# Optimization experiments

Measured on AMD Instinct MI355X. Metric: run time of the kernel, lower is better.

Reference implementation:

```python
import jax, jax.numpy as jnp
import numpy as np

EPS = 1e-8
TAU = 0.2
IOU_THR = 0.5
NEG = -1e9
N, C, H, D_FG, D_CLS = 8192, 1024, 256, 64, 128


def setup_inputs() -> dict:
    key = jax.random.key(0)
    ks = jax.random.split(key, 11)
    def lin(k, fan_in, fan_out):
        return jax.random.normal(k, (fan_in, fan_out), jnp.float32) / np.sqrt(fan_in)
    return {
        "roi_feats": jax.random.normal(ks[0], (N, C), jnp.float32),
        "labels": jax.random.randint(ks[1], (N,), 0, 21, jnp.int32).astype(jnp.int64),
        "ious": jax.random.uniform(ks[2], (N,), jnp.float32),
        "fg_w1": lin(ks[3], C, H), "fg_b1": jnp.zeros((H,), jnp.float32),
        "fg_w2": lin(ks[4], H, D_FG), "fg_b2": jnp.zeros((D_FG,), jnp.float32),
        "cls_w1": lin(ks[5], C, H), "cls_b1": jnp.zeros((H,), jnp.float32),
        "cls_w2": lin(ks[6], H, D_CLS), "cls_b2": jnp.zeros((D_CLS,), jnp.float32),
    }


def _project_normalize(x, w1, b1, w2, b2):
    h = jax.nn.relu(x @ w1 + b1)
    z = h @ w2 + b2
    norm = jnp.maximum(jnp.linalg.norm(z, axis=1, keepdims=True), EPS)
    return z / norm


def _forward(roi_feats, labels, ious, fg_w1, fg_b1, fg_w2, fg_b2, cls_w1, cls_b1, cls_w2, cls_b2):
    n = roi_feats.shape[0]
    z_fg = _project_normalize(roi_feats, fg_w1, fg_b1, fg_w2, fg_b2)
    z_cls = _project_normalize(roi_feats, cls_w1, cls_b1, cls_w2, cls_b2)

    ignore = labels == -1
    fg = (labels > 0) & ~ignore
    iou_weight = jnp.where(ious > IOU_THR, ious, 0.0)
    eye = jnp.eye(n, dtype=bool)

    # ---- fg/bg contrastive (bg_as_negatives_only=True) ----
    sim_fg = (z_fg @ z_fg.T) / TAU                       # [N,N]
    exp_sim = jnp.exp(sim_fg)
    denom = jnp.sum(exp_sim * (~eye).astype(jnp.float32), axis=1)
    pos = (fg & ~ignore)[None, :] & ~eye                 # positives: fg columns, no self
    n_pos = jnp.sum(pos, axis=1)
    numer = jnp.sum(exp_sim * pos.astype(jnp.float32), axis=1)
    # original computes den = denom + EPS then -log((numer+EPS)/(den+EPS))
    loss_i = -jnp.log((numer + EPS) / (denom + 2.0 * EPS))
    valid = (fg & ~ignore) & (n_pos > 0)
    w = iou_weight * valid.astype(jnp.float32)
    loss_fg_bg = jnp.sum(w * loss_i) / (jnp.sum(w) + EPS)

    # ---- class supervised contrastive ----
    sim_cls = (z_cls @ z_cls.T) / TAU
    sim_masked = jnp.where(eye, NEG, sim_cls)
    log_denom = jax.nn.logsumexp(sim_masked, axis=1)     # [N]
    log_p = jnp.where(eye, NEG, sim_cls - log_denom[:, None])
    # pos_mask keeps diagonal (as in original): same label, col not ignore, col label != 0
    posc = (labels[None, :] == labels[:, None]) & (~ignore)[None, :] & (labels[None, :] != 0)
    n_posc = jnp.sum(posc, axis=1).astype(jnp.float32)
    sum_log_p = jnp.sum(log_p * posc.astype(jnp.float32), axis=1)
    valid_c = (fg & ~ignore) & (n_posc > 0) & jnp.isfinite(log_denom)
    Lzi = jnp.where(valid_c, -sum_log_p / (n_posc + EPS), 0.0)
    wc = iou_weight * valid_c.astype(jnp.float32)
    loss_supcon = jnp.sum(wc * Lzi) / (jnp.sum(wc) + EPS)

    return jnp.stack([loss_fg_bg, loss_supcon])


def reference(roi_feats, labels, ious, fg_w1, fg_b1, fg_w2, fg_b2, cls_w1, cls_b1, cls_w2, cls_b2):
    return _forward(roi_feats, labels, ious, fg_w1, fg_b1, fg_w2, fg_b2, cls_w1, cls_b1, cls_w2, cls_b2)
```

## Files before the change

kernel.cpp:

```cpp
#include <hip/hip_runtime.h>


typedef __attribute__((ext_vector_type(8))) short bs8;
typedef __attribute__((ext_vector_type(4))) float f4;

#define MFMA_BF16(a, b, c) __builtin_amdgcn_mfma_f32_16x16x32_bf16((a), (b), (c), 0, 0, 0)

#if defined(__has_builtin)
#if __has_builtin(__builtin_amdgcn_exp2f)
#define EXP2F(x) __builtin_amdgcn_exp2f(x)
#endif
#endif
#ifndef EXP2F
#define EXP2F(x) exp2f(x)
#endif

#define K_LOG2E 7.2134752044448170f

__device__ __forceinline__ unsigned short f2bf(float f) {
  unsigned int u = __float_as_uint(f);
  u = (u + 0x7fffu + ((u >> 16) & 1u)) >> 16;
  return (unsigned short)u;
}
__device__ __forceinline__ float bf2f(unsigned short s) {
  return __uint_as_float(((unsigned int)s) << 16);
}

constexpr size_t O_W1T  = 0;
constexpr size_t O_W2TF = 1048576;
constexpr size_t O_W2TC = 1081344;
constexpr size_t O_H    = 1146880;
constexpr size_t O_ZF   = 9535488;
constexpr size_t O_ZC   = 10584064;
constexpr size_t O_SCLS = 12681216;
constexpr size_t O_ROWD = 12697600;
constexpr size_t O_ROWN = 12730368;
constexpr size_t O_ROWS = 12763136;
constexpr size_t O_SCAL = 12795904;
constexpr size_t O_HIST = 12795920;
constexpr size_t O_NFG  = 12796048;
constexpr int ZERO_WORDS = (int)((O_SCAL + 16 - O_SCLS) / 4);

__global__ void __launch_bounds__(256) prep_kernel(
    const float* __restrict__ fgw1, const float* __restrict__ clsw1,
    const float* __restrict__ fgw2, const float* __restrict__ clsw2,
    const int* __restrict__ labels,
    unsigned short* __restrict__ W1T, unsigned short* __restrict__ W2Tf,
    unsigned short* __restrict__ W2Tc,
    int* __restrict__ hist, int* __restrict__ nfg, float* __restrict__ zp) {
  const int b = blockIdx.x;
  const int t = threadIdx.x;

  if (b >= 141) {
    const int i = (b - 141) * 256 + t;
    if (i < ZERO_WORDS) zp[i] = 0.f;
    return;
  }
  if (b == 140) {
    __shared__ int sh[33];
    if (t < 33) sh[t] = 0;
    __syncthreads();
    for (int it = 0; it < 32; it++) {
      const int lab = labels[it * 256 + t];
      if (lab >= 0 && lab < 32) atomicAdd(&sh[lab], 1);
      if (lab > 0) atomicAdd(&sh[32], 1);
    }
    __syncthreads();
    if (t < 32) hist[t] = sh[t];
    if (t == 32) *nfg = sh[32];
    return;
  }
  int m, tb;
  if (b < 64)       { m = 0; tb = b; }
  else if (b < 128) { m = 1; tb = b - 64; }
  else if (b < 132) { m = 2; tb = b - 128; }
  else              { m = 3; tb = b - 132; }
  __shared__ float tile[64][65];
  const float* src;
  unsigned short* dst;
  int R, C;
  if (m == 0)      { src = fgw1;  dst = W1T;              R = 1024; C = 256; }
  else if (m == 1) { src = clsw1; dst = W1T + 256 * 1024; R = 1024; C = 256; }
  else if (m == 2) { src = fgw2;  dst = W2Tf;             R = 256;  C = 64;  }
  else             { src = clsw2; dst = W2Tc;             R = 256;  C = 128; }
  const int cT = C >> 6;
  const int r0 = (tb / cT) << 6, c0 = (tb % cT) << 6;
  {
    const int rr = t >> 4, cc = (t & 15) << 2;
#pragma unroll
    for (int i = 0; i < 4; i++) {
      float4 v = *(const float4*)(src + (size_t)(r0 + rr + i * 16) * C + c0 + cc);
      tile[rr + i * 16][cc] = v.x; tile[rr + i * 16][cc + 1] = v.y;
      tile[rr + i * 16][cc + 2] = v.z; tile[rr + i * 16][cc + 3] = v.w;
    }
  }
  __syncthreads();
  {
    const int dr = t >> 2, dc = (t & 3) << 4;
    bs8 o0, o1;
#pragma unroll
    for (int j = 0; j < 8; j++) o0[j] = (short)f2bf(tile[dc + j][dr]);
#pragma unroll
    for (int j = 0; j < 8; j++) o1[j] = (short)f2bf(tile[dc + 8 + j][dr]);
    unsigned short* dp = dst + (size_t)(c0 + dr) * R + r0 + dc;
    *(bs8*)dp = o0;
    *(bs8*)(dp + 8) = o1;
  }
}

__global__ void __launch_bounds__(512) gemm1_kernel(
    const float* __restrict__ X, const unsigned short* __restrict__ W1T,
    const float* __restrict__ b1f, const float* __restrict__ b1c,
    unsigned short* __restrict__ H) {
  __shared__ __align__(16) unsigned short lA[64 * 72];
  __shared__ __align__(16) unsigned short lB[128 * 72];
  const int t = threadIdx.x;
  const int w = t >> 6, lane = t & 63, ln = lane & 15, quad = lane >> 4;
  const int wr = (w & 3) * 16, wc = (w >> 2) * 64;
  const int m0 = blockIdx.x * 64, n0 = blockIdx.y * 128;

  const int ar = t >> 3, ac = (t & 7) * 8;
  const int br = t >> 2, bc = (t & 3) * 16;
  const float* xbase = X + (size_t)(m0 + ar) * 1024 + ac;
  const unsigned short* bbase = W1T + (size_t)(n0 + br) * 1024 + bc;

  float4 xa[2];
  bs8 xb[2];
#pragma unroll
  for (int i = 0; i < 2; i++) xa[i] = *(const float4*)(xbase + i * 4);
#pragma unroll
  for (int i = 0; i < 2; i++) xb[i] = *(const bs8*)(bbase + i * 8);

  f4 acc[4];
#pragma unroll
  for (int s = 0; s < 4; s++) acc[s] = (f4){0.f, 0.f, 0.f, 0.f};

  for (int ks = 0; ks < 16; ks++) {
    {
      bs8 av;
      av[0] = (short)f2bf(xa[0].x); av[1] = (short)f2bf(xa[0].y);
      av[2] = (short)f2bf(xa[0].z); av[3] = (short)f2bf(xa[0].w);
      av[4] = (short)f2bf(xa[1].x); av[5] = (short)f2bf(xa[1].y);
      av[6] = (short)f2bf(xa[1].z); av[7] = (short)f2bf(xa[1].w);
      *(bs8*)&lA[ar * 72 + ac] = av;
      unsigned short* bp = &lB[br * 72 + bc];
      *(bs8*)(bp) = xb[0];
      *(bs8*)(bp + 8) = xb[1];
    }
    __syncthreads();
    if (ks < 15) {
      const int k1 = (ks + 1) * 64;
#pragma unroll
      for (int i = 0; i < 2; i++) xa[i] = *(const float4*)(xbase + k1 + i * 4);
#pragma unroll
      for (int i = 0; i < 2; i++) xb[i] = *(const bs8*)(bbase + k1 + i * 8);
    }
#pragma unroll
    for (int kk = 0; kk < 2; kk++) {
      bs8 af = *(const bs8*)&lA[(wr + ln) * 72 + kk * 32 + quad * 8];
#pragma unroll
      for (int s = 0; s < 4; s++) {
        bs8 bf = *(const bs8*)&lB[(wc + s * 16 + ln) * 72 + kk * 32 + quad * 8];
        acc[s] = MFMA_BF16(af, bf, acc[s]);
      }
    }
    __syncthreads();
  }
#pragma unroll
  for (int s = 0; s < 4; s++) {
    const int n = n0 + wc + s * 16 + ln;
    const float b = (n < 256) ? b1f[n] : b1c[n - 256];
#pragma unroll
    for (int r = 0; r < 4; r++) {
      float v = fmaxf(acc[s][r] + b, 0.f);
      H[(size_t)(m0 + wr + quad * 4 + r) * 512 + n] = f2bf(v);
    }
  }
}

__global__ void __launch_bounds__(256) gemm2_kernel(
    const unsigned short* __restrict__ H,
    const unsigned short* __restrict__ W2Tf, const unsigned short* __restrict__ W2Tc,
    const float* __restrict__ b2f, const float* __restrict__ b2c,
    unsigned short* __restrict__ Zf, unsigned short* __restrict__ Zc) {
  const int t = threadIdx.x;
  const int w = t >> 6, lane = t & 63, ln = lane & 15, quad = lane >> 4;
  const int rw = blockIdx.x * 32 + (w & 1) * 16;

  if (w < 2) {
    const unsigned short* hrow = H + (size_t)(rw + ln) * 512;
    f4 acc[4];
#pragma unroll
    for (int s = 0; s < 4; s++) acc[s] = (f4){0.f, 0.f, 0.f, 0.f};
#pragma unroll
    for (int ks = 0; ks < 8; ks++) {
      bs8 af = *(const bs8*)(hrow + ks * 32 + quad * 8);
#pragma unroll
      for (int s = 0; s < 4; s++) {
        bs8 bf = *(const bs8*)(W2Tf + (size_t)(s * 16 + ln) * 256 + ks * 32 + quad * 8);
        acc[s] = MFMA_BF16(af, bf, acc[s]);
      }
    }
    float ss[4] = {0.f, 0.f, 0.f, 0.f};
#pragma unroll
    for (int s = 0; s < 4; s++) {
      float b = b2f[s * 16 + ln];
#pragma unroll
      for (int r = 0; r < 4; r++) {
        acc[s][r] += b;
        ss[r] = fmaf(acc[s][r], acc[s][r], ss[r]);
      }
    }
#pragma unroll
    for (int r = 0; r < 4; r++) {
#pragma unroll
      for (int off = 1; off < 16; off <<= 1) ss[r] += __shfl_xor(ss[r], off, 64);
      float sc = 1.f / fmaxf(sqrtf(ss[r]), 1e-8f);
#pragma unroll
      for (int s = 0; s < 4; s++)
        Zf[(size_t)(rw + quad * 4 + r) * 64 + s * 16 + ln] = f2bf(acc[s][r] * sc);
    }
  } else {
    const unsigned short* hrow = H + (size_t)(rw + ln) * 512 + 256;
    f4 acc[8];
#pragma unroll
    for (int s = 0; s < 8; s++) acc[s] = (f4){0.f, 0.f, 0.f, 0.f};
#pragma unroll
    for (int ks = 0; ks < 8; ks++) {
      bs8 af = *(const bs8*)(hrow + ks * 32 + quad * 8);
#pragma unroll
      for (int s = 0; s < 8; s++) {
        bs8 bf = *(const bs8*)(W2Tc + (size_t)(s * 16 + ln) * 256 + ks * 32 + quad * 8);
        acc[s] = MFMA_BF16(af, bf, acc[s]);
      }
    }
    float ss[4] = {0.f, 0.f, 0.f, 0.f};
#pragma unroll
    for (int s = 0; s < 8; s++) {
      float b = b2c[s * 16 + ln];
#pragma unroll
      for (int r = 0; r < 4; r++) {
        acc[s][r] += b;
        ss[r] = fmaf(acc[s][r], acc[s][r], ss[r]);
      }
    }
#pragma unroll
    for (int r = 0; r < 4; r++) {
#pragma unroll
      for (int off = 1; off < 16; off <<= 1) ss[r] += __shfl_xor(ss[r], off, 64);
      float sc = 1.f / fmaxf(sqrtf(ss[r]), 1e-8f);
#pragma unroll
      for (int s = 0; s < 8; s++)
        Zc[(size_t)(rw + quad * 4 + r) * 128 + s * 16 + ln] = f2bf(acc[s][r] * sc);
    }
  }
}

__global__ void __launch_bounds__(128) scls_kernel(const unsigned short* __restrict__ Zc,
                                                   const int* __restrict__ labels,
                                                   float* __restrict__ Scls) {
  const int c = blockIdx.x + 1;
  const int t = threadIdx.x;
  const int r0 = blockIdx.y * 256;
  float acc = 0.f;
#pragma unroll 4
  for (int r = r0; r < r0 + 256; r++) {
    if (labels[r] == c) acc += bf2f(Zc[(size_t)r * 128 + t]);
  }
  atomicAdd(&Scls[c * 128 + t], acc);
}

__global__ void __launch_bounds__(256) sim2_kernel(
    const unsigned short* __restrict__ Zf, const unsigned short* __restrict__ Zc,
    const int* __restrict__ labels,
    float* __restrict__ rowD, float* __restrict__ rowN, float* __restrict__ rowS) {
  const int bi = blockIdx.x, y = blockIdx.y;
  const bool isfg = (y < 9);
  const int y2 = isfg ? y : y - 9;
  int dlo, dhi;
  if (y2 == 0)      { dlo = 0;      dhi = 3;      }
  else if (y2 < 8)  { dlo = y2 * 4; dhi = y2 * 4 + 3; }
  else              { dlo = 32;     dhi = 32; if (bi >= 32) return; }

  __shared__ __align__(16) char arena[19456];
  const int t = threadIdx.x;
  const int w = t >> 6, lane = t & 63, ln = lane & 15, quad = lane >> 4;
  const int rbase = bi * 128 + w * 32;

  if (isfg) {
    unsigned short* sZf = (unsigned short*)arena;
    float* sFg = (float*)(arena + 9216);
    float* sCol = (float*)(arena + 9472);

    bs8 afg[2][2];
    float fgr[2][4];
#pragma unroll
    for (int rs = 0; rs < 2; rs++) {
      const unsigned short* zf = Zf + (size_t)(rbase + rs * 16 + ln) * 64;
#pragma unroll
      for (int s = 0; s < 2; s++) afg[rs][s] = *(const bs8*)(zf + s * 32 + quad * 8);
#pragma unroll
      for (int r = 0; r < 4; r++)
        fgr[rs][r] = (labels[rbase + rs * 16 + quad * 4 + r] > 0) ? 1.f : 0.f;
    }

    float dacc[2][4] = {}, nacc[2][4] = {};

    for (int d = dlo; d <= dhi; d++) {
      const int bj = (bi + d) & 63;
      float cd[2][4] = {}, cn[2][4] = {};

#pragma unroll
      for (int ct = 0; ct < 2; ct++) {
        const int c0 = bj * 128 + ct * 64;
        __syncthreads();
#pragma unroll
        for (int i = 0; i < 2; i++) {
          int ch = t + i * 256;
          int j = ch >> 3, c8 = (ch & 7) * 8;
          *(bs8*)&sZf[j * 72 + c8] = *(const bs8*)(Zf + (size_t)(c0 + j) * 64 + c8);
        }
        if (t < 64) sFg[t] = (labels[c0 + t] > 0) ? 1.f : 0.f;
        __syncthreads();

#pragma unroll
        for (int s = 0; s < 4; s++) {
          const int lcol = s * 16 + ln;
          const float fgc = sFg[lcol];
          bs8 b0 = *(const bs8*)&sZf[lcol * 72 + quad * 8];
          bs8 b1 = *(const bs8*)&sZf[lcol * 72 + 32 + quad * 8];
#pragma unroll
          for (int rs = 0; rs < 2; rs++) {
            f4 c = {0.f, 0.f, 0.f, 0.f};
            c = MFMA_BF16(afg[rs][0], b0, c);
            c = MFMA_BF16(afg[rs][1], b1, c);
#pragma unroll
            for (int r = 0; r < 4; r++) {
              float e = EXP2F(c[r] * K_LOG2E);
              dacc[rs][r] += e;
              nacc[rs][r] = fmaf(fgc, e, nacc[rs][r]);
              cd[ct][s] += e;
              cn[ct][s] = fmaf(fgr[rs][r], e, cn[ct][s]);
            }
          }
        }
      }

      if (d != 0) {
#pragma unroll
        for (int ct = 0; ct < 2; ct++)
#pragma unroll
          for (int s = 0; s < 4; s++) {
            float dv = cd[ct][s], nv = cn[ct][s];
#pragma unroll
            for (int off = 16; off < 64; off <<= 1) {
              dv += __shfl_xor(dv, off, 64);
              nv += __shfl_xor(nv, off, 64);
            }
            if (quad == 0) {
              const int idx = (((w * 2 + ct) * 4 + s) * 16 + ln) * 2;
              sCol[idx] = dv;
              sCol[idx + 1] = nv;
            }
          }
        __syncthreads();
        if (t < 128) {
          const int ct = t >> 6, s = (t >> 4) & 3, lm = t & 15;
          float dv = 0.f, nv = 0.f;
#pragma unroll
          for (int ww = 0; ww < 4; ww++) {
            const int idx = (((ww * 2 + ct) * 4 + s) * 16 + lm) * 2;
            dv += sCol[idx];
            nv += sCol[idx + 1];
          }
          const int col = bj * 128 + t;
          atomicAdd(&rowD[col], dv);
          atomicAdd(&rowN[col], nv);
        }
      }
    }

#pragma unroll
    for (int rs = 0; rs < 2; rs++)
#pragma unroll
      for (int r = 0; r < 4; r++) {
        float dv = dacc[rs][r], nv = nacc[rs][r];
#pragma unroll
        for (int off = 1; off < 16; off <<= 1) {
          dv += __shfl_xor(dv, off, 64);
          nv += __shfl_xor(nv, off, 64);
        }
        if (ln == 0) {
          int row = rbase + rs * 16 + quad * 4 + r;
          atomicAdd(&rowD[row], dv);
          atomicAdd(&rowN[row], nv);
        }
      }
  } else {
    unsigned short* sZc = (unsigned short*)arena;
    float* sCol = (float*)(arena + 17408);

    bs8 acl[2][4];
#pragma unroll
    for (int rs = 0; rs < 2; rs++) {
      const unsigned short* zc = Zc + (size_t)(rbase + rs * 16 + ln) * 128;
#pragma unroll
      for (int s = 0; s < 4; s++) acl[rs][s] = *(const bs8*)(zc + s * 32 + quad * 8);
    }

    float sacc[2][4] = {};

    for (int d = dlo; d <= dhi; d++) {
      const int bj = (bi + d) & 63;
      float cs[2][4] = {};

#pragma unroll
      for (int ct = 0; ct < 2; ct++) {
        const int c0 = bj * 128 + ct * 64;
        __syncthreads();
#pragma unroll
        for (int i = 0; i < 4; i++) {
          int ch = t + i * 256;
          int j = ch >> 4, c8 = (ch & 15) * 8;
          *(bs8*)&sZc[j * 136 + c8] = *(const bs8*)(Zc + (size_t)(c0 + j) * 128 + c8);
        }
        __syncthreads();

#pragma unroll
        for (int s = 0; s < 4; s++) {
          const int lcol = s * 16 + ln;
          bs8 bc0 = *(const bs8*)&sZc[lcol * 136 + quad * 8];
          bs8 bc1 = *(const bs8*)&sZc[lcol * 136 + 32 + quad * 8];
          bs8 bc2 = *(const bs8*)&sZc[lcol * 136 + 64 + quad * 8];
          bs8 bc3 = *(const bs8*)&sZc[lcol * 136 + 96 + quad * 8];
#pragma unroll
          for (int rs = 0; rs < 2; rs++) {
            f4 c = {0.f, 0.f, 0.f, 0.f};
            c = MFMA_BF16(acl[rs][0], bc0, c);
            c = MFMA_BF16(acl[rs][1], bc1, c);
            c = MFMA_BF16(acl[rs][2], bc2, c);
            c = MFMA_BF16(acl[rs][3], bc3, c);
#pragma unroll
            for (int r = 0; r < 4; r++) {
              float e = EXP2F(c[r] * K_LOG2E);
              sacc[rs][r] += e;
              cs[ct][s] += e;
            }
          }
        }
      }

      if (d != 0) {
#pragma unroll
        for (int ct = 0; ct < 2; ct++)
#pragma unroll
          for (int s = 0; s < 4; s++) {
            float sv = cs[ct][s];
#pragma unroll
            for (int off = 16; off < 64; off <<= 1) sv += __shfl_xor(sv, off, 64);
            if (quad == 0) sCol[((w * 2 + ct) * 4 + s) * 16 + ln] = sv;
          }
        __syncthreads();
        if (t < 128) {
          const int ct = t >> 6, s = (t >> 4) & 3, lm = t & 15;
          float sv = 0.f;
#pragma unroll
          for (int ww = 0; ww < 4; ww++) sv += sCol[((ww * 2 + ct) * 4 + s) * 16 + lm];
          atomicAdd(&rowS[bj * 128 + t], sv);
        }
      }
    }

#pragma unroll
    for (int rs = 0; rs < 2; rs++)
#pragma unroll
      for (int r = 0; r < 4; r++) {
        float sv = sacc[rs][r];
#pragma unroll
        for (int off = 1; off < 16; off <<= 1) sv += __shfl_xor(sv, off, 64);
        if (ln == 0)
          atomicAdd(&rowS[rbase + rs * 16 + quad * 4 + r], sv);
      }
  }
}

__global__ void __launch_bounds__(256) finalize_kernel(
    const unsigned short* __restrict__ Zf, const unsigned short* __restrict__ Zc,
    const int* __restrict__ labels, const float* __restrict__ ious,
    const float* __restrict__ rowD, const float* __restrict__ rowN,
    const float* __restrict__ rowS, const float* __restrict__ Scls,
    const int* __restrict__ hist, const int* __restrict__ nfg,
    float* __restrict__ scal) {
  __shared__ float red[4][4];
  const int t = threadIdx.x, w = t >> 6, lane = t & 63;
  float aw0 = 0.f, al0 = 0.f, aw1 = 0.f, al1 = 0.f;
  const int NFG = *nfg;
  for (int it = 0; it < 16; it++) {
    const int i = it * 512 + blockIdx.x * 4 + w;
    const int lab = labels[i];
    if (lab > 0 && lab < 32) {
      const float iou = ious[i];
      const float iw = (iou > 0.5f) ? iou : 0.f;
      float dot = 0.f, ssq = 0.f;
#pragma unroll
      for (int p = 0; p < 2; p++) {
        const int k = lane + p * 64;
        const float z = bf2f(Zc[(size_t)i * 128 + k]);
        dot = fmaf(z, Scls[lab * 128 + k], dot);
        ssq = fmaf(z, z, ssq);
      }
      float zf = bf2f(Zf[(size_t)i * 64 + lane]);
      float ssqf = zf * zf;
#pragma unroll
      for (int off = 1; off < 64; off <<= 1) {
        dot += __shfl_xor(dot, off, 64);
        ssq += __shfl_xor(ssq, off, 64);
        ssqf += __shfl_xor(ssqf, off, 64);
      }
      if (lane == 0) {
        const float ef = EXP2F(K_LOG2E * ssqf);
        if (NFG - 1 > 0) {
          const float D = rowD[i] - ef;
          const float Nn = rowN[i] - ef;
          const float loss = logf(D + 2e-8f) - logf(Nn + 1e-8f);
          aw0 += iw;
          al0 += iw * loss;
        }
        const int npc = hist[lab];
        if (npc > 0) {
          const float S = rowS[i] - EXP2F(K_LOG2E * ssq);
          const float logden = logf(S);
          const float slp = (dot - ssq) * 5.0f - (float)(npc - 1) * logden - 1e9f;
          aw1 += iw;
          al1 += iw * (-slp / ((float)npc + 1e-8f));
        }
      }
    }
  }
  if (lane == 0) { red[w][0] = aw0; red[w][1] = al0; red[w][2] = aw1; red[w][3] = al1; }
  __syncthreads();
  if (t < 4) atomicAdd(&scal[t], red[0][t] + red[1][t] + red[2][t] + red[3][t]);
}

__global__ void writeout_kernel(const float* __restrict__ scal, float* __restrict__ out) {
  if (threadIdx.x == 0) {
    out[0] = scal[1] / (scal[0] + 1e-8f);
    out[1] = scal[3] / (scal[2] + 1e-8f);
  }
}

extern "C" void kernel_launch(void* const* d_in, const int* in_sizes, int n_in,
                              void* d_out, int out_size, void* d_ws, size_t ws_size,
                              hipStream_t stream) {
  (void)in_sizes; (void)n_in; (void)out_size; (void)ws_size;
  const float* roi    = (const float*)d_in[0];
  const int*   labels = (const int*)d_in[1];
  const float* ious   = (const float*)d_in[2];
  const float* fgw1   = (const float*)d_in[3];
  const float* fgb1   = (const float*)d_in[4];
  const float* fgw2   = (const float*)d_in[5];
  const float* fgb2   = (const float*)d_in[6];
  const float* clsw1  = (const float*)d_in[7];
  const float* clsb1  = (const float*)d_in[8];
  const float* clsw2  = (const float*)d_in[9];
  const float* clsb2  = (const float*)d_in[10];

  char* ws = (char*)d_ws;
  unsigned short* W1T  = (unsigned short*)(ws + O_W1T);
  unsigned short* W2Tf = (unsigned short*)(ws + O_W2TF);
  unsigned short* W2Tc = (unsigned short*)(ws + O_W2TC);
  unsigned short* Hb   = (unsigned short*)(ws + O_H);
  unsigned short* Zf   = (unsigned short*)(ws + O_ZF);
  unsigned short* Zc   = (unsigned short*)(ws + O_ZC);
  float* Scls = (float*)(ws + O_SCLS);
  float* rowD = (float*)(ws + O_ROWD);
  float* rowN = (float*)(ws + O_ROWN);
  float* rowS = (float*)(ws + O_ROWS);
  float* scal = (float*)(ws + O_SCAL);
  int* hist = (int*)(ws + O_HIST);
  int* nfg  = (int*)(ws + O_NFG);
  float* out = (float*)d_out;

  hipLaunchKernelGGL(prep_kernel, dim3(254), dim3(256), 0, stream,
                     fgw1, clsw1, fgw2, clsw2, labels, W1T, W2Tf, W2Tc,
                     hist, nfg, (float*)(ws + O_SCLS));
  hipLaunchKernelGGL(gemm1_kernel, dim3(128, 4), dim3(512), 0, stream,
                     roi, W1T, fgb1, clsb1, Hb);
  hipLaunchKernelGGL(gemm2_kernel, dim3(256), dim3(256), 0, stream,
                     Hb, W2Tf, W2Tc, fgb2, clsb2, Zf, Zc);
  hipLaunchKernelGGL(scls_kernel, dim3(20, 32), dim3(128), 0, stream, Zc, labels, Scls);
  hipLaunchKernelGGL(sim2_kernel, dim3(64, 18), dim3(256), 0, stream,
                     Zf, Zc, labels, rowD, rowN, rowS);
  hipLaunchKernelGGL(finalize_kernel, dim3(128), dim3(256), 0, stream,
                     Zf, Zc, labels, ious, rowD, rowN, rowS, Scls, hist, nfg, scal);
  hipLaunchKernelGGL(writeout_kernel, dim3(1), dim3(64), 0, stream, scal, out);
}
```

Baseline: 205.1 us.

## Fuse class-sum accumulation into gemm2 and final writeout into finalize

Drops the separate scls_kernel: gemm2 now accumulates per-class sums of the normalized Zc rows in shared memory with LDS atomics and flushes nonzero entries to global Scls. It also removes writeout_kernel, using a last-block ticket counter in finalize_kernel to compute the output ratios. This saves two kernel launches and a re-read of Zc, at the cost of LDS atomics inside gemm2 and a counter placed inside the zeroed Scls region (class 31 slot), which depends on prep zeroing it each call.

New measurement: 201.6 us, median of 3. No clear change (-1.7%).

```diff
diff --git a/kernel.cpp b/kernel.cpp
--- a/kernel.cpp
+++ b/kernel.cpp
@@ -39,6 +39,7 @@
 constexpr size_t O_SCAL = 12795904;
 constexpr size_t O_HIST = 12795920;
 constexpr size_t O_NFG  = 12796048;
+constexpr size_t O_CNT  = O_SCLS + 31 * 128 * 4;
 constexpr int ZERO_WORDS = (int)((O_SCAL + 16 - O_SCLS) / 4);
 
 __global__ void __launch_bounds__(256) prep_kernel(
@@ -182,8 +183,14 @@
     const unsigned short* __restrict__ H,
     const unsigned short* __restrict__ W2Tf, const unsigned short* __restrict__ W2Tc,
     const float* __restrict__ b2f, const float* __restrict__ b2c,
-    unsigned short* __restrict__ Zf, unsigned short* __restrict__ Zc) {
+    const int* __restrict__ labels,
+    unsigned short* __restrict__ Zf, unsigned short* __restrict__ Zc,
+    float* __restrict__ Scls) {
+  __shared__ float sS[21 * 128];
   const int t = threadIdx.x;
+  for (int i = t; i < 21 * 128; i += 256) sS[i] = 0.f;
+  __syncthreads();
+
   const int w = t >> 6, lane = t & 63, ln = lane & 15, quad = lane >> 4;
   const int rw = blockIdx.x * 32 + (w & 1) * 16;
 
@@ -249,25 +256,21 @@
 #pragma unroll
       for (int off = 1; off < 16; off <<= 1) ss[r] += __shfl_xor(ss[r], off, 64);
       float sc = 1.f / fmaxf(sqrtf(ss[r]), 1e-8f);
-#pragma unroll
-      for (int s = 0; s < 8; s++)
-        Zc[(size_t)(rw + quad * 4 + r) * 128 + s * 16 + ln] = f2bf(acc[s][r] * sc);
-    }
-  }
-}
-
-__global__ void __launch_bounds__(128) scls_kernel(const unsigned short* __restrict__ Zc,
-                                                   const int* __restrict__ labels,
-                                                   float* __restrict__ Scls) {
-  const int c = blockIdx.x + 1;
-  const int t = threadIdx.x;
-  const int r0 = blockIdx.y * 256;
-  float acc = 0.f;
-#pragma unroll 4
-  for (int r = r0; r < r0 + 256; r++) {
-    if (labels[r] == c) acc += bf2f(Zc[(size_t)r * 128 + t]);
-  }
-  atomicAdd(&Scls[c * 128 + t], acc);
+      const int lab = labels[rw + quad * 4 + r];
+#pragma unroll
+      for (int s = 0; s < 8; s++) {
+        const unsigned short us = f2bf(acc[s][r] * sc);
+        Zc[(size_t)(rw + quad * 4 + r) * 128 + s * 16 + ln] = us;
+        if (lab > 0 && lab < 21) atomicAdd(&sS[lab * 128 + s * 16 + ln], bf2f(us));
+      }
+    }
+  }
+
+  __syncthreads();
+  for (int i = t; i < 20 * 128; i += 256) {
+    const float v = sS[128 + i];
+    if (v != 0.f) atomicAdd(&Scls[128 + i], v);
+  }
 }
 
 __global__ void __launch_bounds__(256) sim2_kernel(
@@ -490,7 +493,8 @@
     const float* __restrict__ rowD, const float* __restrict__ rowN,
     const float* __restrict__ rowS, const float* __restrict__ Scls,
     const int* __restrict__ hist, const int* __restrict__ nfg,
-    float* __restrict__ scal) {
+    float* __restrict__ scal, unsigned int* __restrict__ cnt,
+    float* __restrict__ out) {
   __shared__ float red[4][4];
   const int t = threadIdx.x, w = t >> 6, lane = t & 63;
   float aw0 = 0.f, al0 = 0.f, aw1 = 0.f, al1 = 0.f;
@@ -540,12 +544,19 @@
   if (lane == 0) { red[w][0] = aw0; red[w][1] = al0; red[w][2] = aw1; red[w][3] = al1; }
   __syncthreads();
   if (t < 4) atomicAdd(&scal[t], red[0][t] + red[1][t] + red[2][t] + red[3][t]);
-}
-
-__global__ void writeout_kernel(const float* __restrict__ scal, float* __restrict__ out) {
-  if (threadIdx.x == 0) {
-    out[0] = scal[1] / (scal[0] + 1e-8f);
-    out[1] = scal[3] / (scal[2] + 1e-8f);
+  __syncthreads();
+  if (t == 0) {
+    __threadfence();
+    const unsigned int ticket = atomicAdd(cnt, 1u);
+    if (ticket == gridDim.x - 1) {
+      __threadfence();
+      const float s0 = atomicAdd(&scal[0], 0.f);
+      const float s1 = atomicAdd(&scal[1], 0.f);
+      const float s2 = atomicAdd(&scal[2], 0.f);
+      const float s3 = atomicAdd(&scal[3], 0.f);
+      out[0] = s1 / (s0 + 1e-8f);
+      out[1] = s3 / (s2 + 1e-8f);
+    }
   }
 }
 
@@ -577,6 +588,7 @@
   float* rowN = (float*)(ws + O_ROWN);
   float* rowS = (float*)(ws + O_ROWS);
   float* scal = (float*)(ws + O_SCAL);
+  unsigned int* cnt = (unsigned int*)(ws + O_CNT);
   int* hist = (int*)(ws + O_HIST);
   int* nfg  = (int*)(ws + O_NFG);
   float* out = (float*)d_out;
@@ -587,11 +599,10 @@
   hipLaunchKernelGGL(gemm1_kernel, dim3(128, 4), dim3(512), 0, stream,
                      roi, W1T, fgb1, clsb1, Hb);
   hipLaunchKernelGGL(gemm2_kernel, dim3(256), dim3(256), 0, stream,
-                     Hb, W2Tf, W2Tc, fgb2, clsb2, Zf, Zc);
-  hipLaunchKernelGGL(scls_kernel, dim3(20, 32), dim3(128), 0, stream, Zc, labels, Scls);
+                     Hb, W2Tf, W2Tc, fgb2, clsb2, labels, Zf, Zc, Scls);
   hipLaunchKernelGGL(sim2_kernel, dim3(64, 18), dim3(256), 0, stream,
                      Zf, Zc, labels, rowD, rowN, rowS);
   hipLaunchKernelGGL(finalize_kernel, dim3(128), dim3(256), 0, stream,
-                     Zf, Zc, labels, ious, rowD, rowN, rowS, Scls, hist, nfg, scal);
-  hipLaunchKernelGGL(writeout_kernel, dim3(1), dim3(64), 0, stream, scal, out);
-}
+                     Zf, Zc, labels, ious, rowD, rowN, rowS, Scls, hist, nfg,
+                     scal, cnt, out);
+}
```
